# Performance work log

Hardware: AMD Instinct MI355X
Metric: run time of the kernel (lower is better)

The kernel has to match this reference:

```python
import jax, jax.numpy as jnp
import numpy as np
import math

B, S, D, H = 2, 2048, 1024, 16
HD = D // H  # head dim = 64


def setup_inputs() -> dict:
    key = jax.random.key(0)
    k1, k2, k3, k4, k5 = jax.random.split(key, 5)
    query = jax.random.normal(k1, (B, S, D), dtype=jnp.float32)
    # tail padding: sequence lengths 1536 and 1792 -> positions >= length are padded (True)
    lengths = jnp.array([1536, 1792], dtype=jnp.int32)
    padding_mask = jnp.arange(S, dtype=jnp.int32)[None, :] >= lengths[:, None]  # [B,S] bool
    qkv_w = jax.random.normal(k2, (3 * D, D), dtype=jnp.float32) * 0.02
    qkv_b = jax.random.uniform(k3, (3 * D,), dtype=jnp.float32, minval=-0.03, maxval=0.03)
    out_w = jax.random.normal(k4, (D, D), dtype=jnp.float32) * 0.02
    out_b = jax.random.uniform(k5, (D,), dtype=jnp.float32, minval=-0.03, maxval=0.03)
    return {"query": query, "padding_mask": padding_mask,
            "qkv_w": qkv_w, "qkv_b": qkv_b, "out_w": out_w, "out_b": out_b}


def reference(query, padding_mask, qkv_w, qkv_b, out_w, out_b):
    # self-attention path (qkv_same=True): fused qkv projection then split
    qkv = query @ qkv_w.T + qkv_b                      # [B,S,3D]
    q, k, v = jnp.split(qkv, 3, axis=-1)               # each [B,S,D]

    def split_heads(x):
        return x.reshape(B, S, H, HD).transpose(0, 2, 1, 3)  # [B,H,S,HD]

    q, k, v = split_heads(q), split_heads(k), split_heads(v)

    # scores scaled by sqrt(head_dim)
    w = jnp.einsum('bhqd,bhkd->bhqk', q, k) / math.sqrt(HD)  # [B,H,S,S]

    # causal (future) mask: strict upper triangle masked
    future = jnp.triu(jnp.ones((S, S), dtype=bool), 1)
    w = jnp.where(future[None, None, :, :], -jnp.inf, w)
    # key padding mask
    w = jnp.where(padding_mask[:, None, None, :], -jnp.inf, w)

    a = jax.nn.softmax(w, axis=-1)
    # rows of fully-padded sequences are zeroed (dropout is identity in eval)
    all_masked = jnp.all(padding_mask, axis=-1)        # [B]
    a = jnp.where(all_masked[:, None, None, None], 0.0, a)

    x = jnp.einsum('bhqk,bhkd->bhqd', a, v)            # [B,H,S,HD]
    x = x.transpose(0, 2, 1, 3).reshape(B, S, D)       # merge heads
    return x @ out_w.T + out_b
```

## Files before the change

### kernel.cpp

```cpp
#include <hip/hip_runtime.h>
#include <hip/hip_bf16.h>
#include <stdint.h>

#define S_  2048
#define B_  2
#define H_  16
#define D_  1024
#define HD_ 64

typedef short short8 __attribute__((ext_vector_type(8)));
typedef float f32x4  __attribute__((ext_vector_type(4)));
typedef float f32x16 __attribute__((ext_vector_type(16)));

__device__ __forceinline__ unsigned short bf16_rne(float f) {
  unsigned int u = __float_as_uint(f);
  u += 0x7fffu + ((u >> 16) & 1u);
  return (unsigned short)(u >> 16);
}

__device__ __forceinline__ f32x4 mfma_bf16(short8 a, short8 b, f32x4 c) {
  return __builtin_amdgcn_mfma_f32_16x16x32_bf16(a, b, c, 0, 0, 0);
}

__device__ __forceinline__ f32x16 mfma32(short8 a, short8 b, f32x16 c) {
  return __builtin_amdgcn_mfma_f32_32x32x16_bf16(a, b, c, 0, 0, 0);
}

__device__ __forceinline__ unsigned int cvtpk_bf16(float lo, float hi) {
  unsigned int r;
  asm("v_cvt_pk_bf16_f32 %0, %1, %2" : "=v"(r) : "v"(lo), "v"(hi));
  return r;
}

__global__ void cvt3_kernel(const float* __restrict__ a, unsigned short* __restrict__ oa, int na8,
                            const float* __restrict__ b, unsigned short* __restrict__ ob, int nb8,
                            const float* __restrict__ c, unsigned short* __restrict__ oc, int nc8) {
  int i = blockIdx.x * blockDim.x + threadIdx.x;
  const float* in; unsigned short* out; int idx;
  if (i < na8) { in = a; out = oa; idx = i; }
  else if (i < na8 + nb8) { in = b; out = ob; idx = i - na8; }
  else if (i < na8 + nb8 + nc8) { in = c; out = oc; idx = i - na8 - nb8; }
  else return;
  const float4* p = (const float4*)in + (size_t)idx * 2;
  float4 x = p[0], y = p[1];
  union { unsigned short u[8]; short8 v; } r;
  r.u[0] = bf16_rne(x.x); r.u[1] = bf16_rne(x.y);
  r.u[2] = bf16_rne(x.z); r.u[3] = bf16_rne(x.w);
  r.u[4] = bf16_rne(y.x); r.u[5] = bf16_rne(y.y);
  r.u[6] = bf16_rne(y.z); r.u[7] = bf16_rne(y.w);
  *((short8*)out + idx) = r.v;
}

__global__ void lengths_kernel(const void* __restrict__ mask, int* __restrict__ lens) {
  __shared__ int mn[B_];
  __shared__ int anyb;
  int t = threadIdx.x;
  if (t < B_) mn[t] = S_;
  if (t == 0) anyb = 0;
  __syncthreads();
  const unsigned char* mb = (const unsigned char*)mask;
  for (int i = t; i < B_ * S_; i += 256) {
    if (mb[i]) { anyb = 1; atomicMin(&mn[i >> 11], i & (S_ - 1)); }
  }
  __syncthreads();
  if (!anyb) {
    const int* mi = (const int*)mask;
    for (int i = t; i < B_ * S_; i += 256) {
      if (mi[i]) atomicMin(&mn[i >> 11], i & (S_ - 1));
    }
    __syncthreads();
  }
  if (t < B_) lens[t] = mn[t];
}

__global__ __launch_bounds__(512, 2) void gemm8p_kernel(
    const unsigned short* __restrict__ A,
    const unsigned short* __restrict__ W,
    int K, int NBX,
    const float* __restrict__ bias,
    unsigned short* __restrict__ qb,
    unsigned short* __restrict__ kb,
    unsigned short* __restrict__ vb) {
  __shared__ __align__(16) unsigned short lds[65536];

  const int nwg = gridDim.x;
  const int cpx = nwg >> 3;
  const int bid = blockIdx.x;
  const int virt = (bid & 7) * cpx + (bid >> 3);
  const int bx = virt % NBX, by = virt / NBX;
  const int tile_m = by * 256, tile_n = bx * 256;
  const int t = threadIdx.x;
  const int lane = t & 63, w = t >> 6;
  const int wm = w >> 2, wn = w & 3;
  const int l15 = lane & 15, lk = lane >> 4;
  const int NT = K >> 6;

  f32x4 acc[8][4];
#pragma unroll
  for (int i = 0; i < 8; i++)
#pragma unroll
    for (int j = 0; j < 4; j++) { f32x4 z = {0.f, 0.f, 0.f, 0.f}; acc[i][j] = z; }

  const int L0 = t, L1 = 512 + t;
  const int r0 = L0 >> 3, c0 = (L0 & 7) ^ (r0 & 7);
  const int r1 = L1 >> 3, c1 = (L1 & 7) ^ (r1 & 7);

#define STAGE_HALF(SRC, GROW0, DSTE, KC)                                      \
  {                                                                           \
    __builtin_amdgcn_global_load_lds(                                         \
        (const __attribute__((address_space(1))) void*)(                      \
            (SRC) + (size_t)((GROW0) + r0) * K + (KC) + c0 * 8),              \
        (__attribute__((address_space(3))) void*)(&lds[(DSTE) + L0 * 8]),     \
        16, 0, 0);                                                            \
    __builtin_amdgcn_global_load_lds(                                         \
        (const __attribute__((address_space(1))) void*)(                      \
            (SRC) + (size_t)((GROW0) + r1) * K + (KC) + c1 * 8),              \
        (__attribute__((address_space(3))) void*)(&lds[(DSTE) + L1 * 8]),     \
        16, 0, 0);                                                            \
  }

  STAGE_HALF(A, tile_m,        0,    0);
  STAGE_HALF(W, tile_n,        32768, 0);
  STAGE_HALF(A, tile_m + 128,  8192, 0);
  STAGE_HALF(W, tile_n + 128,  32768 + 8192, 0);
  asm volatile("s_waitcnt vmcnt(4)" ::: "memory");
  __builtin_amdgcn_s_barrier();

  for (int tc = 0; tc < NT; ++tc) {
    const int cb = (tc & 1) * 16384;
    const int ob = ((tc & 1) ^ 1) * 16384;
    int tn = tc + 1; if (tn >= NT) tn = NT - 1;
    const int k0n = tn << 6;

#pragma unroll
    for (int p = 0; p < 4; ++p) {
      const int mh = (p & 1);
      const int nh = (p >> 1);
      short8 af[4][2], bfr[2][2];
#pragma unroll
      for (int fi = 0; fi < 4; ++fi) {
        const int rl = fi * 32 + wm * 16 + l15;
#pragma unroll
        for (int ks = 0; ks < 2; ++ks) {
          const int sw = (ks * 4 + lk) ^ (rl & 7);
          af[fi][ks] = *(const short8*)&lds[cb + mh * 8192 + rl * 64 + sw * 8];
        }
      }
#pragma unroll
      for (int fj = 0; fj < 2; ++fj) {
        const int cl = wn * 32 + fj * 16 + l15;
#pragma unroll
        for (int ks = 0; ks < 2; ++ks) {
          const int sw = (ks * 4 + lk) ^ (cl & 7);
          bfr[fj][ks] =
              *(const short8*)&lds[32768 + cb + nh * 8192 + cl * 64 + sw * 8];
        }
      }
      if (p == 0)      STAGE_HALF(A, tile_m,       ob,                k0n)
      else if (p == 1) STAGE_HALF(W, tile_n,       32768 + ob,        k0n)
      else if (p == 2) STAGE_HALF(A, tile_m + 128, ob + 8192,         k0n)
      else             STAGE_HALF(W, tile_n + 128, 32768 + ob + 8192, k0n);
      if (p != 2) asm volatile("s_waitcnt vmcnt(4)" ::: "memory");
      else        asm volatile("" ::: "memory");
      __builtin_amdgcn_s_barrier();
      asm volatile("s_waitcnt lgkmcnt(0)" ::: "memory");
      __builtin_amdgcn_s_setprio(1);
#pragma unroll
      for (int fi = 0; fi < 4; ++fi)
#pragma unroll
        for (int fj = 0; fj < 2; ++fj)
#pragma unroll
          for (int ks = 0; ks < 2; ++ks)
            acc[mh * 4 + fi][nh * 2 + fj] =
                mfma_bf16(af[fi][ks], bfr[fj][ks], acc[mh * 4 + fi][nh * 2 + fj]);
      __builtin_amdgcn_s_setprio(0);
      __builtin_amdgcn_s_barrier();
    }
  }
  asm volatile("s_waitcnt vmcnt(0)" ::: "memory");
#undef STAGE_HALF

#pragma unroll
  for (int j = 0; j < 4; ++j) {
    const int gn = tile_n + (j >> 1) * 128 + wn * 32 + (j & 1) * 16 + l15;
    const float bv = bias[gn];
    const int which = gn >> 10, dd = gn & (D_ - 1);
    const int h = dd >> 6, d = dd & 63;
    unsigned short* dstp = (which == 0) ? qb : (which == 1) ? kb : vb;
    const float mul = (which == 0) ? 0.125f : 1.0f;
#pragma unroll
    for (int i = 0; i < 8; ++i) {
      const int gmb = tile_m + (i >> 2) * 128 + (i & 3) * 32 + wm * 16 + lk * 4;
#pragma unroll
      for (int r = 0; r < 4; ++r) {
        const int gm = gmb + r;
        const int bb = gm >> 11, s = gm & (S_ - 1);
        dstp[((size_t)((bb * H_ + h) * S_ + s)) * HD_ + d] =
            bf16_rne((acc[i][j][r] + bv) * mul);
      }
    }
  }
}

__global__ __launch_bounds__(256) void gemm_bt_kernel(
    const unsigned short* __restrict__ A,
    const unsigned short* __restrict__ W,
    int K, int N,
    const float* __restrict__ bias,
    float* __restrict__ outf) {
  __shared__ unsigned short As[128 * 32];
  __shared__ unsigned short Bs[128 * 32];
  const int tile_m = blockIdx.y * 128;
  const int tile_n = blockIdx.x * 128;
  const int t = threadIdx.x;
  const int lane = t & 63;
  const int w = t >> 6;
  const int wr = w >> 1, wc = w & 1;
  const int l15 = lane & 15, lk = lane >> 4;

  f32x4 acc[4][4];
#pragma unroll
  for (int i = 0; i < 4; i++)
#pragma unroll
    for (int j = 0; j < 4; j++) { f32x4 z = {0.f, 0.f, 0.f, 0.f}; acc[i][j] = z; }

  for (int k0 = 0; k0 < K; k0 += 32) {
#pragma unroll
    for (int c = 0; c < 2; ++c) {
      int e = (c * 256 + t) * 8;
      int row = e >> 5, col = e & 31;
      __builtin_amdgcn_global_load_lds(
          (__attribute__((address_space(1))) void*)(A + (size_t)(tile_m + row) * K + k0 + col),
          (__attribute__((address_space(3))) void*)(&As[e]), 16, 0, 0);
      __builtin_amdgcn_global_load_lds(
          (__attribute__((address_space(1))) void*)(W + (size_t)(tile_n + row) * K + k0 + col),
          (__attribute__((address_space(3))) void*)(&Bs[e]), 16, 0, 0);
    }
    asm volatile("s_waitcnt vmcnt(0)" ::: "memory");
    __syncthreads();

    short8 af[4], bfr[4];
#pragma unroll
    for (int i = 0; i < 4; i++)
      af[i] = *(const short8*)&As[(wr * 64 + i * 16 + l15) * 32 + lk * 8];
#pragma unroll
    for (int j = 0; j < 4; j++)
      bfr[j] = *(const short8*)&Bs[(wc * 64 + j * 16 + l15) * 32 + lk * 8];
#pragma unroll
    for (int i = 0; i < 4; i++)
#pragma unroll
      for (int j = 0; j < 4; j++)
        acc[i][j] = mfma_bf16(af[i], bfr[j], acc[i][j]);
    __syncthreads();
  }

#pragma unroll
  for (int i = 0; i < 4; i++) {
#pragma unroll
    for (int j = 0; j < 4; j++) {
      int gn = tile_n + wc * 64 + j * 16 + l15;
      float bv = bias[gn];
#pragma unroll
      for (int r = 0; r < 4; r++) {
        int gm = tile_m + wr * 64 + i * 16 + lk * 4 + r;
        outf[(size_t)gm * N + gn] = acc[i][j][r] + bv;
      }
    }
  }
}

__global__ __launch_bounds__(256, 3) void attn_kernel(
    const unsigned short* __restrict__ qbuf,
    const unsigned short* __restrict__ kbuf,
    const unsigned short* __restrict__ vbuf,
    const int* __restrict__ lens,
    unsigned short* __restrict__ attn_out) {
  __shared__ __align__(16) char smem[33792];
  __shared__ float lsh[2][64];

  const int bid = blockIdx.x;
  const int xcd = bid & 7, nn = bid >> 3;
  const int rr = nn >> 5, cc = nn & 31;
  const int bh = (xcd << 2) | (cc & 3);
  const int qlo = cc >> 2;
  const int qt = (rr & 1) ? (8 * rr + 7 - qlo) : (8 * rr + qlo);
  const int b = bh >> 4;
  const int len = lens[b];
  const int t = threadIdx.x;
  const int lane = t & 63, w = t >> 6;
  const int g = w >> 1, wq = w & 1;
  const int l31 = lane & 31, hi = lane >> 5;
  const int hi8 = hi * 8, hi4 = hi * 4;
  const int q0 = qt * 64 + wq * 32;
  const int qme = q0 + l31;

  unsigned short* Ks = (unsigned short*)(smem + g * 8192);
  unsigned int*   Vt = (unsigned int*)(smem + 16384 + g * 8704);

  const unsigned short* qbh = qbuf + (size_t)bh * S_ * HD_;
  const unsigned short* kbh = kbuf + (size_t)bh * S_ * HD_;
  const unsigned short* vbh = vbuf + (size_t)bh * S_ * HD_;

  short8 qf[4];
#pragma unroll
  for (int ds = 0; ds < 4; ++ds)
    qf[ds] = *(const short8*)&qbh[(size_t)(q0 + l31) * HD_ + ds * 16 + hi8];

  f32x16 o[2] = {{}, {}};
  float rsum = 0.f;

  const int ke = (len - 1) >> 6;
  const int kt_end = qt < ke ? qt : ke;
  const int NI = (kt_end >> 1) + 1;

  const int tg = t & 127;
  const int kr0 = tg >> 3, kc0 = tg & 7;
  const int vr2 = tg & 31, vcb = (tg >> 5) << 1;

  short8 pk[4], pva0 = {}, pva1 = {}, pvb0 = {}, pvb1 = {};
#pragma unroll
  for (int m = 0; m < 4; ++m) pk[m] = pva0;

#define LDG(KT)                                                               \
  {                                                                           \
    int ks_ = (KT) * 64;                                                      \
    pk[0] = *(const short8*)&kbh[(size_t)(ks_ + kr0     ) * HD_ + kc0 * 8];   \
    pk[1] = *(const short8*)&kbh[(size_t)(ks_ + kr0 + 16) * HD_ + kc0 * 8];   \
    pk[2] = *(const short8*)&kbh[(size_t)(ks_ + kr0 + 32) * HD_ + kc0 * 8];   \
    pk[3] = *(const short8*)&kbh[(size_t)(ks_ + kr0 + 48) * HD_ + kc0 * 8];   \
    const unsigned short* vp = vbh + (size_t)(ks_ + 2 * vr2) * HD_ + vcb * 8; \
    pva0 = *(const short8*)vp;       pva1 = *(const short8*)(vp + HD_);       \
    pvb0 = *(const short8*)(vp + 8); pvb1 = *(const short8*)(vp + HD_ + 8);   \
  }

  int my_kt = g;
  bool act = (my_kt <= kt_end);
  if (act) LDG(my_kt);

  typedef union { unsigned int u[4]; short8 s; } pa_t;

  for (int i = 0; i < NI; ++i) {
    __syncthreads();
    if (act) {
#pragma unroll
      for (int m = 0; m < 4; ++m) {
        const int r = kr0 + 16 * m;
        *(short8*)&Ks[r * 64 + ((kc0 ^ (r & 7)) << 3)] = pk[m];
      }
#pragma unroll
      for (int j = 0; j < 8; ++j) {
        unsigned int w0 = (unsigned int)(unsigned short)pva0[j] |
                          ((unsigned int)(unsigned short)pva1[j] << 16);
        unsigned int w1 = (unsigned int)(unsigned short)pvb0[j] |
                          ((unsigned int)(unsigned short)pvb1[j] << 16);
        Vt[(vcb * 8 + j) * 34 + vr2] = w0;
        Vt[((vcb + 1) * 8 + j) * 34 + vr2] = w1;
      }
    }
    __syncthreads();
    const int nxt = my_kt + 2;
    const bool nact = (nxt <= kt_end);
    if (nact) LDG(nxt);

    const int ks0 = my_kt * 64;
    if (act && ks0 <= q0 + 31) {
      const bool needM = (ks0 + 63 >= q0) || (ks0 + 63 >= len);
      const bool dokb1 = (ks0 + 32 <= q0 + 31) && (ks0 + 32 < len);

      pa_t pa[4];
      {
        f32x16 s0 = {};
#pragma unroll
        for (int ds = 0; ds < 4; ++ds) {
          const int cg = ((ds << 1) | hi) ^ (l31 & 7);
          const short8 kf = *(const short8*)&Ks[l31 * 64 + (cg << 3)];
          s0 = mfma32(kf, qf[ds], s0);
        }
        float pr[16];
#pragma unroll
        for (int r = 0; r < 16; ++r) {
          const int crow = (r & 3) + 8 * (r >> 2) + hi4;
          float p = __expf(s0[r]);
          if (needM) {
            const int key = ks0 + crow;
            if (key > qme || key >= len) p = 0.f;
          }
          pr[r] = p; rsum += p;
        }
        unsigned int A0 = cvtpk_bf16(pr[0], pr[1]);
        unsigned int A1 = cvtpk_bf16(pr[2], pr[3]);
        unsigned int B0 = cvtpk_bf16(pr[4], pr[5]);
        unsigned int B1 = cvtpk_bf16(pr[6], pr[7]);
        asm volatile("v_permlane32_swap_b32 %0, %1" : "+v"(A0), "+v"(B0));
        asm volatile("v_permlane32_swap_b32 %0, %1" : "+v"(A1), "+v"(B1));
        pa[0].u[0] = A0; pa[0].u[1] = A1; pa[0].u[2] = B0; pa[0].u[3] = B1;
        unsigned int C0 = cvtpk_bf16(pr[8], pr[9]);
        unsigned int C1 = cvtpk_bf16(pr[10], pr[11]);
        unsigned int D0 = cvtpk_bf16(pr[12], pr[13]);
        unsigned int D1 = cvtpk_bf16(pr[14], pr[15]);
        asm volatile("v_permlane32_swap_b32 %0, %1" : "+v"(C0), "+v"(D0));
        asm volatile("v_permlane32_swap_b32 %0, %1" : "+v"(C1), "+v"(D1));
        pa[1].u[0] = C0; pa[1].u[1] = C1; pa[1].u[2] = D0; pa[1].u[3] = D1;
      }
      if (dokb1) {
        f32x16 s1 = {};
#pragma unroll
        for (int ds = 0; ds < 4; ++ds) {
          const int cg = ((ds << 1) | hi) ^ (l31 & 7);
          const short8 kf = *(const short8*)&Ks[(32 + l31) * 64 + (cg << 3)];
          s1 = mfma32(kf, qf[ds], s1);
        }
        float pr[16];
#pragma unroll
        for (int r = 0; r < 16; ++r) {
          const int crow = 32 + (r & 3) + 8 * (r >> 2) + hi4;
          float p = __expf(s1[r]);
          if (needM) {
            const int key = ks0 + crow;
            if (key > qme || key >= len) p = 0.f;
          }
          pr[r] = p; rsum += p;
        }
        unsigned int A0 = cvtpk_bf16(pr[0], pr[1]);
        unsigned int A1 = cvtpk_bf16(pr[2], pr[3]);
        unsigned int B0 = cvtpk_bf16(pr[4], pr[5]);
        unsigned int B1 = cvtpk_bf16(pr[6], pr[7]);
        asm volatile("v_permlane32_swap_b32 %0, %1" : "+v"(A0), "+v"(B0));
        asm volatile("v_permlane32_swap_b32 %0, %1" : "+v"(A1), "+v"(B1));
        pa[2].u[0] = A0; pa[2].u[1] = A1; pa[2].u[2] = B0; pa[2].u[3] = B1;
        unsigned int C0 = cvtpk_bf16(pr[8], pr[9]);
        unsigned int C1 = cvtpk_bf16(pr[10], pr[11]);
        unsigned int D0 = cvtpk_bf16(pr[12], pr[13]);
        unsigned int D1 = cvtpk_bf16(pr[14], pr[15]);
        asm volatile("v_permlane32_swap_b32 %0, %1" : "+v"(C0), "+v"(D0));
        asm volatile("v_permlane32_swap_b32 %0, %1" : "+v"(C1), "+v"(D1));
        pa[3].u[0] = C0; pa[3].u[1] = C1; pa[3].u[2] = D0; pa[3].u[3] = D1;
      }
#pragma unroll
      for (int dh = 0; dh < 2; ++dh) {
        const int vbase = (dh * 32 + l31) * 34 + hi4;
#pragma unroll
        for (int ks = 0; ks < 4; ++ks) {
          if (ks >= 2 && !dokb1) continue;
          uint2 va = *(const uint2*)&Vt[vbase + 8 * ks];
          uint2 vb2 = *(const uint2*)&Vt[vbase + 8 * ks + 2];
          pa_t vv;
          vv.u[0] = va.x; vv.u[1] = va.y; vv.u[2] = vb2.x; vv.u[3] = vb2.y;
          o[dh] = mfma32(pa[ks].s, vv.s, o[dh]);
        }
      }
    }
    my_kt = nxt; act = nact;
  }
#undef LDG

  rsum += __shfl_xor(rsum, 32, 64);

  float* mo = (float*)smem;
  __syncthreads();
  if (g == 1) {
#pragma unroll
    for (int r = 0; r < 16; ++r) {
      const int qb = wq * 32 + (r & 3) + 8 * (r >> 2) + hi4;
      mo[qb * 66 + l31]      = o[0][r];
      mo[qb * 66 + 32 + l31] = o[1][r];
    }
    if (hi == 0) lsh[1][wq * 32 + l31] = rsum;
  }
  __syncthreads();
  if (g == 0) {
    const float lt = rsum + lsh[1][wq * 32 + l31];
    const float inv = (lt > 0.f) ? (1.0f / lt) : 0.f;
    if (hi == 0) lsh[0][wq * 32 + l31] = inv;
#pragma unroll
    for (int r = 0; r < 16; ++r) {
      const int cr = (r & 3) + 8 * (r >> 2) + hi4;
      const int qb = wq * 32 + cr;
      const float iv = lsh[0][wq * 32 + cr];
      const int s = qt * 64 + qb;
      unsigned short* op =
          &attn_out[((size_t)(b * S_ + s)) * D_ + (bh & 15) * HD_ + l31];
      op[0]  = bf16_rne((o[0][r] + mo[qb * 66 + l31]) * iv);
      op[32] = bf16_rne((o[1][r] + mo[qb * 66 + 32 + l31]) * iv);
    }
  }
}

extern "C" void kernel_launch(void* const* d_in, const int* in_sizes, int n_in,
                              void* d_out, int out_size, void* d_ws, size_t ws_size,
                              hipStream_t stream) {
  const float* query = (const float*)d_in[0];
  const void*  mask  = d_in[1];
  const float* qkv_w = (const float*)d_in[2];
  const float* qkv_b = (const float*)d_in[3];
  const float* out_w = (const float*)d_in[4];
  const float* out_b = (const float*)d_in[5];
  float* out = (float*)d_out;

  char* ws = (char*)d_ws;
  unsigned short* qx     = (unsigned short*)(ws);
  unsigned short* wqkv   = (unsigned short*)(ws + (8u  << 20));
  unsigned short* wout   = (unsigned short*)(ws + (14u << 20));
  unsigned short* qbuf   = (unsigned short*)(ws + (16u << 20));
  unsigned short* kbuf   = (unsigned short*)(ws + (24u << 20));
  unsigned short* vbuf   = (unsigned short*)(ws + (32u << 20));
  unsigned short* attn_o = qx;
  int* lens              = (int*)(ws + (40u << 20));

  lengths_kernel<<<1, 256, 0, stream>>>(mask, lens);
  const int na8 = B_ * S_ * D_ / 8, nb8 = 3 * D_ * D_ / 8, nc8 = D_ * D_ / 8;
  cvt3_kernel<<<(na8 + nb8 + nc8) / 256, 256, 0, stream>>>(
      query, qx, na8, qkv_w, wqkv, nb8, out_w, wout, nc8);

  gemm8p_kernel<<<192, 512, 0, stream>>>(qx, wqkv, D_, 3 * D_ / 256, qkv_b,
                                         qbuf, kbuf, vbuf);

  attn_kernel<<<1024, 256, 0, stream>>>(qbuf, kbuf, vbuf, lens, attn_o);

  dim3 g2(D_ / 128, B_ * S_ / 128);
  gemm_bt_kernel<<<g2, 256, 0, stream>>>(attn_o, wout, D_, D_, out_b, out);
}
```

Baseline: 136.5 us.

## Merge lengths into convert kernel, double-buffer output GEMM, use exp2 softmax

The separate mask-length kernel is folded into block 0 of the conversion kernel, which removes one launch. The output-projection GEMM now double-buffers its LDS tiles so the global-to-LDS load of the next K slice overlaps the current MFMAs, and it raises wave priority around the MFMA block. The Q scale now includes log2(e) so the attention softmax can use exp2f instead of __expf. Block 0 of the conversion kernel now does serial extra work, and exp2f may lower to a slower, more exact path than the hardware exp2.

```diff
diff --git a/kernel.cpp b/kernel.cpp
--- a/kernel.cpp
+++ b/kernel.cpp
@@ -34,7 +34,29 @@
 
 __global__ void cvt3_kernel(const float* __restrict__ a, unsigned short* __restrict__ oa, int na8,
                             const float* __restrict__ b, unsigned short* __restrict__ ob, int nb8,
-                            const float* __restrict__ c, unsigned short* __restrict__ oc, int nc8) {
+                            const float* __restrict__ c, unsigned short* __restrict__ oc, int nc8,
+                            const void* __restrict__ mask, int* __restrict__ lens) {
+  if (blockIdx.x == 0) {
+    __shared__ int mn[B_];
+    __shared__ int anyb;
+    int tt = threadIdx.x;
+    if (tt < B_) mn[tt] = S_;
+    if (tt == 0) anyb = 0;
+    __syncthreads();
+    const unsigned char* mb = (const unsigned char*)mask;
+    for (int i = tt; i < B_ * S_; i += 256) {
+      if (mb[i]) { anyb = 1; atomicMin(&mn[i >> 11], i & (S_ - 1)); }
+    }
+    __syncthreads();
+    if (!anyb) {
+      const int* mi = (const int*)mask;
+      for (int i = tt; i < B_ * S_; i += 256) {
+        if (mi[i]) atomicMin(&mn[i >> 11], i & (S_ - 1));
+      }
+      __syncthreads();
+    }
+    if (tt < B_) lens[tt] = mn[tt];
+  }
   int i = blockIdx.x * blockDim.x + threadIdx.x;
   const float* in; unsigned short* out; int idx;
   if (i < na8) { in = a; out = oa; idx = i; }
@@ -51,28 +73,6 @@
   *((short8*)out + idx) = r.v;
 }
 
-__global__ void lengths_kernel(const void* __restrict__ mask, int* __restrict__ lens) {
-  __shared__ int mn[B_];
-  __shared__ int anyb;
-  int t = threadIdx.x;
-  if (t < B_) mn[t] = S_;
-  if (t == 0) anyb = 0;
-  __syncthreads();
-  const unsigned char* mb = (const unsigned char*)mask;
-  for (int i = t; i < B_ * S_; i += 256) {
-    if (mb[i]) { anyb = 1; atomicMin(&mn[i >> 11], i & (S_ - 1)); }
-  }
-  __syncthreads();
-  if (!anyb) {
-    const int* mi = (const int*)mask;
-    for (int i = t; i < B_ * S_; i += 256) {
-      if (mi[i]) atomicMin(&mn[i >> 11], i & (S_ - 1));
-    }
-    __syncthreads();
-  }
-  if (t < B_) lens[t] = mn[t];
-}
-
 __global__ __launch_bounds__(512, 2) void gemm8p_kernel(
     const unsigned short* __restrict__ A,
     const unsigned short* __restrict__ W,
@@ -187,7 +187,7 @@
     const int which = gn >> 10, dd = gn & (D_ - 1);
     const int h = dd >> 6, d = dd & 63;
     unsigned short* dstp = (which == 0) ? qb : (which == 1) ? kb : vb;
-    const float mul = (which == 0) ? 0.125f : 1.0f;
+    const float mul = (which == 0) ? 0.18033688011112042f : 1.0f;
 #pragma unroll
     for (int i = 0; i < 8; ++i) {
       const int gmb = tile_m + (i >> 2) * 128 + (i & 3) * 32 + wm * 16 + lk * 4;
@@ -208,8 +208,8 @@
     int K, int N,
     const float* __restrict__ bias,
     float* __restrict__ outf) {
-  __shared__ unsigned short As[128 * 32];
-  __shared__ unsigned short Bs[128 * 32];
+  __shared__ unsigned short As[2][128 * 32];
+  __shared__ unsigned short Bs[2][128 * 32];
   const int tile_m = blockIdx.y * 128;
   const int tile_n = blockIdx.x * 128;
   const int t = threadIdx.x;
@@ -217,6 +217,7 @@
   const int w = t >> 6;
   const int wr = w >> 1, wc = w & 1;
   const int l15 = lane & 15, lk = lane >> 4;
+  const int NT = K >> 5;
 
   f32x4 acc[4][4];
 #pragma unroll
@@ -224,35 +225,53 @@
 #pragma unroll
     for (int j = 0; j < 4; j++) { f32x4 z = {0.f, 0.f, 0.f, 0.f}; acc[i][j] = z; }
 
-  for (int k0 = 0; k0 < K; k0 += 32) {
-#pragma unroll
-    for (int c = 0; c < 2; ++c) {
-      int e = (c * 256 + t) * 8;
-      int row = e >> 5, col = e & 31;
-      __builtin_amdgcn_global_load_lds(
-          (__attribute__((address_space(1))) void*)(A + (size_t)(tile_m + row) * K + k0 + col),
-          (__attribute__((address_space(3))) void*)(&As[e]), 16, 0, 0);
-      __builtin_amdgcn_global_load_lds(
-          (__attribute__((address_space(1))) void*)(W + (size_t)(tile_n + row) * K + k0 + col),
-          (__attribute__((address_space(3))) void*)(&Bs[e]), 16, 0, 0);
-    }
+#define STAGE_BT(BUF, KC)                                                     \
+  {                                                                           \
+    _Pragma("unroll")                                                         \
+    for (int c = 0; c < 2; ++c) {                                             \
+      int e = (c * 256 + t) * 8;                                              \
+      int row = e >> 5, col = e & 31;                                         \
+      __builtin_amdgcn_global_load_lds(                                       \
+          (const __attribute__((address_space(1))) void*)(                    \
+              A + (size_t)(tile_m + row) * K + (KC) + col),                   \
+          (__attribute__((address_space(3))) void*)(&As[BUF][e]), 16, 0, 0);  \
+      __builtin_amdgcn_global_load_lds(                                       \
+          (const __attribute__((address_space(1))) void*)(                    \
+              W + (size_t)(tile_n + row) * K + (KC) + col),                   \
+          (__attribute__((address_space(3))) void*)(&Bs[BUF][e]), 16, 0, 0);  \
+    }                                                                         \
+  }
+
+  STAGE_BT(0, 0);
+  asm volatile("s_waitcnt vmcnt(0)" ::: "memory");
+  __syncthreads();
+
+  int cur = 0;
+  for (int tc = 0; tc < NT; ++tc) {
+    if (tc + 1 < NT) STAGE_BT(cur ^ 1, (tc + 1) << 5);
+
+    const unsigned short* Ac = As[cur];
+    const unsigned short* Bc = Bs[cur];
+    short8 af[4], bfr[4];
+#pragma unroll
+    for (int i = 0; i < 4; i++)
+      af[i] = *(const short8*)&Ac[(wr * 64 + i * 16 + l15) * 32 + lk * 8];
+#pragma unroll
+    for (int j = 0; j < 4; j++)
+      bfr[j] = *(const short8*)&Bc[(wc * 64 + j * 16 + l15) * 32 + lk * 8];
+    __builtin_amdgcn_s_setprio(1);
+#pragma unroll
+    for (int i = 0; i < 4; i++)
+#pragma unroll
+      for (int j = 0; j < 4; j++)
+        acc[i][j] = mfma_bf16(af[i], bfr[j], acc[i][j]);
+    __builtin_amdgcn_s_setprio(0);
+
     asm volatile("s_waitcnt vmcnt(0)" ::: "memory");
     __syncthreads();
-
-    short8 af[4], bfr[4];
-#pragma unroll
-    for (int i = 0; i < 4; i++)
-      af[i] = *(const short8*)&As[(wr * 64 + i * 16 + l15) * 32 + lk * 8];
-#pragma unroll
-    for (int j = 0; j < 4; j++)
-      bfr[j] = *(const short8*)&Bs[(wc * 64 + j * 16 + l15) * 32 + lk * 8];
-#pragma unroll
-    for (int i = 0; i < 4; i++)
-#pragma unroll
-      for (int j = 0; j < 4; j++)
-        acc[i][j] = mfma_bf16(af[i], bfr[j], acc[i][j]);
-    __syncthreads();
-  }
+    cur ^= 1;
+  }
+#undef STAGE_BT
 
 #pragma unroll
   for (int i = 0; i < 4; i++) {
@@ -380,7 +399,7 @@
 #pragma unroll
         for (int r = 0; r < 16; ++r) {
           const int crow = (r & 3) + 8 * (r >> 2) + hi4;
-          float p = __expf(s0[r]);
+          float p = exp2f(s0[r]);
           if (needM) {
             const int key = ks0 + crow;
             if (key > qme || key >= len) p = 0.f;
@@ -414,7 +433,7 @@
 #pragma unroll
         for (int r = 0; r < 16; ++r) {
           const int crow = 32 + (r & 3) + 8 * (r >> 2) + hi4;
-          float p = __expf(s1[r]);
+          float p = exp2f(s1[r]);
           if (needM) {
             const int key = ks0 + crow;
             if (key > qme || key >= len) p = 0.f;
@@ -507,10 +526,9 @@
   unsigned short* attn_o = qx;
   int* lens              = (int*)(ws + (40u << 20));
 
-  lengths_kernel<<<1, 256, 0, stream>>>(mask, lens);
   const int na8 = B_ * S_ * D_ / 8, nb8 = 3 * D_ * D_ / 8, nc8 = D_ * D_ / 8;
   cvt3_kernel<<<(na8 + nb8 + nc8) / 256, 256, 0, stream>>>(
-      query, qx, na8, qkv_w, wqkv, nb8, out_w, wout, nc8);
+      query, qx, na8, qkv_w, wqkv, nb8, out_w, wout, nc8, mask, lens);
 
   gemm8p_kernel<<<192, 512, 0, stream>>>(qx, wqkv, D_, 3 * D_ / 256, qkv_b,
                                          qbuf, kbuf, vbuf);
```

Result: no change. 138.5 us (+1.5%).
